# Performance work log

Measured on AMD Instinct MI355X. Metric: run time of the kernel, lower is better.

The kernel has to match this reference:

```python
import jax, jax.numpy as jnp
import numpy as np

E, H, I, T, K = 8, 2048, 768, 1024, 2


def setup_inputs() -> dict:
    key = jax.random.key(0)
    k1, k2, k3, k4, k5 = jax.random.split(key, 5)
    hidden_states = jax.random.normal(k1, (T, H), jnp.float32)
    routing_weights = jax.random.uniform(k2, (T, K), jnp.float32)
    selected_experts = jax.random.randint(k3, (T, K), 0, E, jnp.int32)
    gate_up_proj = jax.random.normal(k4, (E, H, 2 * I), jnp.float32) * 0.02
    down_proj = jax.random.normal(k5, (E, I, H), jnp.float32) * 0.02
    return {
        "hidden_states": hidden_states,
        "routing_weights": routing_weights,
        "gate_up_proj": gate_up_proj,
        "down_proj": down_proj,
        "selected_experts": selected_experts,
    }


def _grouped_gemm(x, w, expert_ids):
    # x: [N, k], w: [E, k, d], expert_ids: [N] (sorted by expert).
    # Dense-masked grouped GEMM: accumulate each expert's masked matmul.
    n = x.shape[0]
    acc0 = jnp.zeros((n, w.shape[-1]), x.dtype)

    def step(acc, ew):
        e, we = ew
        xm = jnp.where((expert_ids == e)[:, None], x, jnp.zeros((), x.dtype))
        return acc + xm @ we, None

    acc, _ = jax.lax.scan(step, acc0, (jnp.arange(w.shape[0]), w))
    return acc


def reference(hidden_states, routing_weights, gate_up_proj, down_proj, selected_experts):
    t, h = hidden_states.shape
    k = selected_experts.shape[1]
    flat = selected_experts.reshape(-1)                     # [T*K]
    sort_idx = jnp.argsort(flat)                            # stable sort by expert id (permute)
    token_idx = sort_idx // k                               # source token per permuted row
    permuted = hidden_states[token_idx]                     # [T*K, H]
    experts_sorted = flat[sort_idx]                         # [T*K]

    fc1 = _grouped_gemm(permuted, gate_up_proj, experts_sorted)   # [T*K, 2I]
    a, b = jnp.split(fc1, 2, axis=-1)
    act = jax.nn.silu(a) * b                                # npu_swiglu
    fc2 = _grouped_gemm(act, down_proj, experts_sorted)     # [T*K, H]

    inv = jnp.argsort(sort_idx)                             # unpermute map (row_ids_map)
    unperm = fc2[inv].reshape(t, k, h)                      # [T, K, H]
    return jnp.einsum('tkh,tk->th', unperm, routing_weights)
```

## Files before the change

### kernel.cpp

```cpp
#include <hip/hip_runtime.h>
#include <math.h>

#define E_  8
#define H_  2048
#define I_  768
#define T_  1024
#define K_  2
#define TK_ 2048
#define GU_ 1536

typedef __bf16 bf16x8 __attribute__((ext_vector_type(8)));
typedef float  f32x4  __attribute__((ext_vector_type(4)));

static __device__ __forceinline__ short f2bf(float f) {
  union { float f; unsigned u; } v; v.f = f;
  unsigned r = (v.u + 0x7fffu + ((v.u >> 16) & 1u)) >> 16;
  return (short)r;
}

static __device__ __forceinline__ unsigned pk2bf(float a, float b) {
  unsigned ua = __float_as_uint(a) + 0x8000u;
  unsigned ub = __float_as_uint(b) + 0x8000u;
  return __builtin_amdgcn_perm(ub, ua, 0x07060302u);
}

#define GLOAD_LDS16(g, l)                                                   \
  __builtin_amdgcn_global_load_lds(                                         \
      (const __attribute__((address_space(1))) void*)(g),                   \
      (__attribute__((address_space(3))) void*)(l), 16, 0, 0)

#define MFMA_BF16_16x16x32 __builtin_amdgcn_mfma_f32_16x16x32_bf16

static __device__ __forceinline__ bf16x8 frag_ld(const unsigned short* base,
                                                 int row, int oct) {
  return *(const bf16x8*)(base + row * 64 + ((oct ^ (row & 7)) * 8));
}

static __device__ __forceinline__ bf16x8 bfrag_ld(const unsigned short* base,
                                                  int n, int o) {
  int phys = (o ^ (n & 7) ^ (n >> 3)) & 7;
  return *(const bf16x8*)(base + n * 64 + phys * 8);
}

#define STEP(IT, G)                                                         \
  do {                                                                      \
    asm volatile("s_waitcnt vmcnt(4)" ::: "memory");                        \
    __builtin_amdgcn_s_barrier();                                           \
    __builtin_amdgcn_sched_barrier(0);                                      \
    int k1_ = ((IT) + 1 < niter ? (IT) + 1 : niter - 1) * 64;               \
    int k3_ = ((IT) + 3 < niter ? (IT) + 3 : niter - 1) * 64;               \
    issueA(cur ^ 1, k1_);                                                   \
    __builtin_amdgcn_sched_barrier(0);                                      \
    const unsigned short* a_ = &As[cur][0];                                 \
    const unsigned short* b_ = &Bs[cur][0];                                 \
    __builtin_amdgcn_s_setprio(1);                                          \
    _Pragma("unroll")                                                       \
    for (int kk = 0; kk < 2; ++kk) {                                        \
      int o = kk * 4 + qf;                                                  \
      bf16x8 af0 = frag_ld(a_, w * 32 + m,      o);                         \
      bf16x8 af1 = frag_ld(a_, w * 32 + 16 + m, o);                         \
      bf16x8 b0  = bfrag_ld(b_, m,      o);                                 \
      bf16x8 b1  = bfrag_ld(b_, 16 + m, o);                                 \
      bf16x8 b2  = bfrag_ld(b_, 32 + m, o);                                 \
      bf16x8 b3  = bfrag_ld(b_, 48 + m, o);                                 \
      acc[0][0] = MFMA_BF16_16x16x32(af0, b0, acc[0][0], 0, 0, 0);          \
      acc[0][1] = MFMA_BF16_16x16x32(af0, b1, acc[0][1], 0, 0, 0);          \
      acc[0][2] = MFMA_BF16_16x16x32(af0, b2, acc[0][2], 0, 0, 0);          \
      acc[0][3] = MFMA_BF16_16x16x32(af0, b3, acc[0][3], 0, 0, 0);          \
      acc[1][0] = MFMA_BF16_16x16x32(af1, b0, acc[1][0], 0, 0, 0);          \
      acc[1][1] = MFMA_BF16_16x16x32(af1, b1, acc[1][1], 0, 0, 0);          \
      acc[1][2] = MFMA_BF16_16x16x32(af1, b2, acc[1][2], 0, 0, 0);          \
      acc[1][3] = MFMA_BF16_16x16x32(af1, b3, acc[1][3], 0, 0, 0);          \
    }                                                                       \
    __builtin_amdgcn_s_setprio(0);                                          \
    writeB(cur ^ 1, G);                                                     \
    loadB(G, k3_);                                                          \
    asm volatile("s_waitcnt lgkmcnt(0)" ::: "memory");                      \
    __builtin_amdgcn_sched_barrier(0);                                      \
    cur ^= 1;                                                               \
  } while (0)

__global__ __launch_bounds__(256) void prep_kernel(
    const float* __restrict__ X, unsigned short* __restrict__ Xb,
    float* __restrict__ out,
    const int* __restrict__ sel, int* __restrict__ offs,
    int* __restrict__ rows, int* __restrict__ inv, int zero_out) {
  __shared__ int cnt[E_], cur[E_], loff[E_ + 1];
  if (blockIdx.x < 2048) {
    int i = blockIdx.x * 256 + threadIdx.x;
    float4 v = ((const float4*)X)[i];
    unsigned p0 = pk2bf(v.x, v.y), p1 = pk2bf(v.z, v.w);
    ((uint2*)Xb)[i] = make_uint2(p0, p1);
    if (zero_out) ((float4*)out)[i] = make_float4(0.f, 0.f, 0.f, 0.f);
    return;
  }
  int t = threadIdx.x;
  if (t < E_) { cnt[t] = 0; cur[t] = 0; }
  __syncthreads();
  for (int p = t; p < TK_; p += 256) atomicAdd(&cnt[sel[p]], 1);
  __syncthreads();
  if (t == 0) {
    int s = 0;
    for (int e = 0; e < E_; ++e) { loff[e] = s; s += cnt[e]; }
    loff[E_] = s;
  }
  __syncthreads();
  if (t <= E_) offs[t] = loff[t];
  for (int p = t; p < TK_; p += 256) {
    int e = sel[p];
    int pos = loff[e] + atomicAdd(&cur[e], 1);
    rows[pos] = p;
    inv[p] = pos;
  }
}

__global__ __launch_bounds__(256, 3) void fc1_mfma(
    const unsigned short* __restrict__ Xb, const float* __restrict__ GUP,
    const int* __restrict__ offs, const int* __restrict__ rows,
    unsigned short* __restrict__ act) {
  __shared__ __align__(16) unsigned short As[2][128 * 64];
  __shared__ __align__(16) unsigned short Bs[2][64 * 64];

  int e    = blockIdx.y >> 4;
  int rbeg = offs[e], rend = offs[e + 1];
  int row0 = rbeg + (blockIdx.y & 15) * 128;
  if (row0 >= rend) return;
  int c0 = blockIdx.x * 32;

  int tid = threadIdx.x, lane = tid & 63, w = tid >> 6;
  int rl  = lane >> 3;
  int oct = (lane & 7) ^ rl;

  const unsigned short* agp[4];
#pragma unroll
  for (int i = 0; i < 4; ++i) {
    int arow = row0 + w * 32 + i * 8 + rl;
    int aidx = arow < rend ? arow : rend - 1;
    agp[i] = Xb + (size_t)(rows[aidx] >> 1) * H_ + oct * 8;
  }
  auto issueA = [&](int buf, int k0) {
#pragma unroll
    for (int i = 0; i < 4; ++i)
      GLOAD_LDS16(agp[i] + k0, &As[buf][0] + (w * 32 + i * 8) * 64);
  };

  int kt = tid >> 4, nt = tid & 15;
  int gbase = (nt < 8) ? (c0 + nt * 4) : (I_ + c0 + (nt - 8) * 4);
  const float* gupe = GUP + (size_t)e * H_ * GU_ + gbase;

  auto loadB = [&](float4 (&vb)[4], int k0) {
#pragma unroll
    for (int i = 0; i < 4; ++i)
      vb[i] = *(const float4*)(gupe + (size_t)(k0 + kt * 4 + i) * GU_);
  };
  auto writeB = [&](int buf, const float4 (&vb)[4]) {
#pragma unroll
    for (int j = 0; j < 4; ++j) {
      int n = nt * 4 + j;
      unsigned u0 = pk2bf(((const float*)&vb[0])[j], ((const float*)&vb[1])[j]);
      unsigned u1 = pk2bf(((const float*)&vb[2])[j], ((const float*)&vb[3])[j]);
      int phys = ((kt >> 1) ^ (n & 7) ^ (n >> 3)) & 7;
      *(uint2*)(&Bs[buf][0] + n * 64 + phys * 8 + (kt & 1) * 4) =
          make_uint2(u0, u1);
    }
  };

  int m = lane & 15, qf = lane >> 4;
  f32x4 acc[2][4] = {};
  float4 vbA[4], vbB[4];

  issueA(0, 0);
  __builtin_amdgcn_sched_barrier(0);
  loadB(vbA, 0);
  writeB(0, vbA);
  loadB(vbA, 64);
  loadB(vbB, 128);
  asm volatile("s_waitcnt lgkmcnt(0)" ::: "memory");
  __builtin_amdgcn_sched_barrier(0);

  const int niter = H_ / 64;
  int cur = 0;
#pragma unroll 1
  for (int it = 0; it < niter; it += 2) {
    STEP(it,     vbA);
    STEP(it + 1, vbB);
  }
  asm volatile("s_waitcnt vmcnt(0)" ::: "memory");

#pragma unroll
  for (int mt = 0; mt < 2; ++mt)
#pragma unroll
    for (int g = 0; g < 2; ++g)
#pragma unroll
      for (int r = 0; r < 4; ++r) {
        int prow = row0 + w * 32 + mt * 16 + qf * 4 + r;
        if (prow < rend) {
          float gv = acc[mt][g][r], uv = acc[mt][g + 2][r];
          float a = gv / (1.0f + __expf(-gv)) * uv;
          act[(size_t)prow * I_ + c0 + g * 16 + m] = (unsigned short)f2bf(a);
        }
      }
}

__global__ __launch_bounds__(256, 3) void fc2_mfma(
    const unsigned short* __restrict__ act, const float* __restrict__ DWN,
    const float* __restrict__ RW,
    const int* __restrict__ offs, const int* __restrict__ rows,
    float* __restrict__ stage, float* __restrict__ out, int use_stage) {
  __shared__ __align__(16) unsigned short As[2][128 * 64];
  __shared__ __align__(16) unsigned short Bs[2][64 * 64];

  int e    = blockIdx.y >> 4;
  int rbeg = offs[e], rend = offs[e + 1];
  int row0 = rbeg + (blockIdx.y & 15) * 128;
  if (row0 >= rend) return;
  int c0 = blockIdx.x * 64;

  int tid = threadIdx.x, lane = tid & 63, w = tid >> 6;
  int rl  = lane >> 3;
  int oct = (lane & 7) ^ rl;

  const unsigned short* agp[4];
#pragma unroll
  for (int i = 0; i < 4; ++i) {
    int arow = row0 + w * 32 + i * 8 + rl;
    int aidx = arow < rend ? arow : rend - 1;
    agp[i] = act + (size_t)aidx * I_ + oct * 8;
  }
  auto issueA = [&](int buf, int k0) {
#pragma unroll
    for (int i = 0; i < 4; ++i)
      GLOAD_LDS16(agp[i] + k0, &As[buf][0] + (w * 32 + i * 8) * 64);
  };

  int kt = tid >> 4, nt = tid & 15;
  const float* dwe = DWN + (size_t)e * I_ * H_ + c0 + nt * 4;

  auto loadB = [&](float4 (&vb)[4], int k0) {
#pragma unroll
    for (int i = 0; i < 4; ++i)
      vb[i] = *(const float4*)(dwe + (size_t)(k0 + kt * 4 + i) * H_);
  };
  auto writeB = [&](int buf, const float4 (&vb)[4]) {
#pragma unroll
    for (int j = 0; j < 4; ++j) {
      int n = nt * 4 + j;
      unsigned u0 = pk2bf(((const float*)&vb[0])[j], ((const float*)&vb[1])[j]);
      unsigned u1 = pk2bf(((const float*)&vb[2])[j], ((const float*)&vb[3])[j]);
      int phys = ((kt >> 1) ^ (n & 7) ^ (n >> 3)) & 7;
      *(uint2*)(&Bs[buf][0] + n * 64 + phys * 8 + (kt & 1) * 4) =
          make_uint2(u0, u1);
    }
  };

  int m = lane & 15, qf = lane >> 4;
  f32x4 acc[2][4] = {};
  float4 vbA[4], vbB[4];

  issueA(0, 0);
  __builtin_amdgcn_sched_barrier(0);
  loadB(vbA, 0);
  writeB(0, vbA);
  loadB(vbA, 64);
  loadB(vbB, 128);
  asm volatile("s_waitcnt lgkmcnt(0)" ::: "memory");
  __builtin_amdgcn_sched_barrier(0);

  const int niter = I_ / 64;
  int cur = 0;
#pragma unroll 1
  for (int it = 0; it < niter; it += 2) {
    STEP(it,     vbA);
    STEP(it + 1, vbB);
  }
  asm volatile("s_waitcnt vmcnt(0)" ::: "memory");

#pragma unroll
  for (int mt = 0; mt < 2; ++mt)
#pragma unroll
    for (int r = 0; r < 4; ++r) {
      int prow = row0 + w * 32 + mt * 16 + qf * 4 + r;
      if (prow < rend) {
        int pair = rows[prow];
        float rw = RW[pair];
        if (use_stage) {
          float* srow = stage + (size_t)prow * H_ + c0 + m;
          srow[0]  = rw * acc[mt][0][r];
          srow[16] = rw * acc[mt][1][r];
          srow[32] = rw * acc[mt][2][r];
          srow[48] = rw * acc[mt][3][r];
        } else {
          float* orow = out + (size_t)(pair >> 1) * H_ + c0 + m;
#pragma unroll
          for (int ntile = 0; ntile < 4; ++ntile)
            atomicAdd(orow + ntile * 16, rw * acc[mt][ntile][r]);
        }
      }
    }
}

__global__ __launch_bounds__(256) void combine_kernel(
    const float* __restrict__ stage, const int* __restrict__ inv,
    float* __restrict__ out) {
  int idx = blockIdx.x * 256 + threadIdx.x;
  int t  = idx >> 9;
  int q  = idx & 511;
  int2 pp = *(const int2*)(inv + 2 * t);
  float4 a = ((const float4*)(stage + (size_t)pp.x * H_))[q];
  float4 b = ((const float4*)(stage + (size_t)pp.y * H_))[q];
  ((float4*)out)[idx] = make_float4(a.x + b.x, a.y + b.y, a.z + b.z, a.w + b.w);
}

extern "C" void kernel_launch(void* const* d_in, const int* in_sizes, int n_in,
                              void* d_out, int out_size, void* d_ws, size_t ws_size,
                              hipStream_t stream) {
  const float* X   = (const float*)d_in[0];
  const float* RW  = (const float*)d_in[1];
  const float* GUP = (const float*)d_in[2];
  const float* DWN = (const float*)d_in[3];
  const int*   SEL = (const int*)d_in[4];
  float* out = (float*)d_out;

  char* ws = (char*)d_ws;
  int* offs = (int*)ws;
  int* rows = (int*)(ws + 1024);
  int* inv  = (int*)(ws + 16384);

  const size_t stage_bytes = (size_t)TK_ * H_ * 4;
  const size_t act_bytes   = (size_t)TK_ * I_ * 2;
  const size_t need_stage  = 32768 + stage_bytes + act_bytes;

  int use_stage = (ws_size >= need_stage) ? 1 : 0;
  unsigned short *Xb, *act;
  float* stage;
  if (use_stage) {
    stage = (float*)(ws + 32768);
    Xb    = (unsigned short*)(ws + 32768);
    act   = (unsigned short*)(ws + 32768 + stage_bytes);
  } else {
    stage = (float*)(ws + 32768);
    Xb    = (unsigned short*)(ws + 32768);
    act   = (unsigned short*)(ws + 32768 + 4194304);
  }

  hipLaunchKernelGGL(prep_kernel, dim3(2049), dim3(256), 0, stream,
                     X, Xb, out, SEL, offs, rows, inv, use_stage ? 0 : 1);
  hipLaunchKernelGGL(fc1_mfma, dim3(24, 128), dim3(256), 0, stream,
                     Xb, GUP, offs, rows, act);
  hipLaunchKernelGGL(fc2_mfma, dim3(32, 128), dim3(256), 0, stream,
                     act, DWN, RW, offs, rows, stage, out, use_stage);
  if (use_stage)
    hipLaunchKernelGGL(combine_kernel, dim3(2048), dim3(256), 0, stream,
                       stage, inv, out);
}
```

Measured before the change: 251.1 us.

## Widen fc2 tile to 128 columns with single B prefetch buffer

The fc2 grouped GEMM tile grows from 128x64 to 128x128 output columns. Each block now does twice the MFMA work per A tile, which halves the reloads of activation rows across column blocks and halves the grid. The double-register B prefetch is replaced by a single 8-float4 buffer with a new step macro and a different vmcnt wait. Occupancy drops from 3 to 2 blocks per CU, and register and LDS pressure rise.

```diff
diff --git a/kernel.cpp b/kernel.cpp
--- a/kernel.cpp
+++ b/kernel.cpp
@@ -80,6 +80,38 @@
     cur ^= 1;                                                               \
   } while (0)
 
+#define STEP2(IT)                                                           \
+  do {                                                                      \
+    asm volatile("s_waitcnt vmcnt(8)" ::: "memory");                        \
+    __builtin_amdgcn_s_barrier();                                           \
+    __builtin_amdgcn_sched_barrier(0);                                      \
+    int k1_ = ((IT) + 1 < niter ? (IT) + 1 : niter - 1) * 64;               \
+    int k2_ = ((IT) + 2 < niter ? (IT) + 2 : niter - 1) * 64;               \
+    issueA(cur ^ 1, k1_);                                                   \
+    __builtin_amdgcn_sched_barrier(0);                                      \
+    const unsigned short* a_ = &As[cur][0];                                 \
+    const unsigned short* b_ = &Bs[cur][0];                                 \
+    __builtin_amdgcn_s_setprio(1);                                          \
+    _Pragma("unroll")                                                       \
+    for (int kk = 0; kk < 2; ++kk) {                                        \
+      int o = kk * 4 + qf;                                                  \
+      bf16x8 af0 = frag_ld(a_, w * 32 + m,      o);                         \
+      bf16x8 af1 = frag_ld(a_, w * 32 + 16 + m, o);                         \
+      _Pragma("unroll")                                                     \
+      for (int j = 0; j < 8; ++j) {                                         \
+        bf16x8 bj = bfrag_ld(b_, j * 16 + m, o);                            \
+        acc[0][j] = MFMA_BF16_16x16x32(af0, bj, acc[0][j], 0, 0, 0);        \
+        acc[1][j] = MFMA_BF16_16x16x32(af1, bj, acc[1][j], 0, 0, 0);        \
+      }                                                                     \
+    }                                                                       \
+    __builtin_amdgcn_s_setprio(0);                                          \
+    writeB(cur ^ 1, vb);                                                    \
+    loadB(vb, k2_);                                                         \
+    asm volatile("s_waitcnt lgkmcnt(0)" ::: "memory");                      \
+    __builtin_amdgcn_sched_barrier(0);                                      \
+    cur ^= 1;                                                               \
+  } while (0)
+
 __global__ __launch_bounds__(256) void prep_kernel(
     const float* __restrict__ X, unsigned short* __restrict__ Xb,
     float* __restrict__ out,
@@ -202,19 +234,19 @@
       }
 }
 
-__global__ __launch_bounds__(256, 3) void fc2_mfma(
+__global__ __launch_bounds__(256, 2) void fc2_mfma(
     const unsigned short* __restrict__ act, const float* __restrict__ DWN,
     const float* __restrict__ RW,
     const int* __restrict__ offs, const int* __restrict__ rows,
     float* __restrict__ stage, float* __restrict__ out, int use_stage) {
   __shared__ __align__(16) unsigned short As[2][128 * 64];
-  __shared__ __align__(16) unsigned short Bs[2][64 * 64];
+  __shared__ __align__(16) unsigned short Bs[2][128 * 64];
 
   int e    = blockIdx.y >> 4;
   int rbeg = offs[e], rend = offs[e + 1];
   int row0 = rbeg + (blockIdx.y & 15) * 128;
   if (row0 >= rend) return;
-  int c0 = blockIdx.x * 64;
+  int c0 = blockIdx.x * 128;
 
   int tid = threadIdx.x, lane = tid & 63, w = tid >> 6;
   int rl  = lane >> 3;
@@ -236,42 +268,44 @@
   int kt = tid >> 4, nt = tid & 15;
   const float* dwe = DWN + (size_t)e * I_ * H_ + c0 + nt * 4;
 
-  auto loadB = [&](float4 (&vb)[4], int k0) {
-#pragma unroll
-    for (int i = 0; i < 4; ++i)
-      vb[i] = *(const float4*)(dwe + (size_t)(k0 + kt * 4 + i) * H_);
-  };
-  auto writeB = [&](int buf, const float4 (&vb)[4]) {
-#pragma unroll
-    for (int j = 0; j < 4; ++j) {
-      int n = nt * 4 + j;
-      unsigned u0 = pk2bf(((const float*)&vb[0])[j], ((const float*)&vb[1])[j]);
-      unsigned u1 = pk2bf(((const float*)&vb[2])[j], ((const float*)&vb[3])[j]);
-      int phys = ((kt >> 1) ^ (n & 7) ^ (n >> 3)) & 7;
-      *(uint2*)(&Bs[buf][0] + n * 64 + phys * 8 + (kt & 1) * 4) =
-          make_uint2(u0, u1);
+  auto loadB = [&](float4 (&vb)[8], int k0) {
+#pragma unroll
+    for (int i = 0; i < 4; ++i) {
+      vb[i]     = *(const float4*)(dwe + (size_t)(k0 + kt * 4 + i) * H_);
+      vb[4 + i] = *(const float4*)(dwe + (size_t)(k0 + kt * 4 + i) * H_ + 64);
     }
   };
+  auto writeB = [&](int buf, const float4 (&vb)[8]) {
+#pragma unroll
+    for (int h = 0; h < 2; ++h)
+#pragma unroll
+      for (int j = 0; j < 4; ++j) {
+        int n = h * 64 + nt * 4 + j;
+        unsigned u0 = pk2bf(((const float*)&vb[h*4+0])[j], ((const float*)&vb[h*4+1])[j]);
+        unsigned u1 = pk2bf(((const float*)&vb[h*4+2])[j], ((const float*)&vb[h*4+3])[j]);
+        int phys = ((kt >> 1) ^ (n & 7) ^ (n >> 3)) & 7;
+        *(uint2*)(&Bs[buf][0] + n * 64 + phys * 8 + (kt & 1) * 4) =
+            make_uint2(u0, u1);
+      }
+  };
 
   int m = lane & 15, qf = lane >> 4;
-  f32x4 acc[2][4] = {};
-  float4 vbA[4], vbB[4];
+  f32x4 acc[2][8] = {};
+  float4 vb[8];
 
   issueA(0, 0);
   __builtin_amdgcn_sched_barrier(0);
-  loadB(vbA, 0);
-  writeB(0, vbA);
-  loadB(vbA, 64);
-  loadB(vbB, 128);
+  loadB(vb, 0);
+  writeB(0, vb);
+  loadB(vb, 64);
   asm volatile("s_waitcnt lgkmcnt(0)" ::: "memory");
   __builtin_amdgcn_sched_barrier(0);
 
   const int niter = I_ / 64;
   int cur = 0;
 #pragma unroll 1
-  for (int it = 0; it < niter; it += 2) {
-    STEP(it,     vbA);
-    STEP(it + 1, vbB);
+  for (int it = 0; it < niter; ++it) {
+    STEP2(it);
   }
   asm volatile("s_waitcnt vmcnt(0)" ::: "memory");
 
@@ -281,19 +315,17 @@
     for (int r = 0; r < 4; ++r) {
       int prow = row0 + w * 32 + mt * 16 + qf * 4 + r;
       if (prow < rend) {
-        int pair = rows[prow];
-        float rw = RW[pair];
+        int pairid = rows[prow];
+        float rw = RW[pairid];
         if (use_stage) {
           float* srow = stage + (size_t)prow * H_ + c0 + m;
-          srow[0]  = rw * acc[mt][0][r];
-          srow[16] = rw * acc[mt][1][r];
-          srow[32] = rw * acc[mt][2][r];
-          srow[48] = rw * acc[mt][3][r];
+#pragma unroll
+          for (int j = 0; j < 8; ++j) srow[j * 16] = rw * acc[mt][j][r];
         } else {
-          float* orow = out + (size_t)(pair >> 1) * H_ + c0 + m;
-#pragma unroll
-          for (int ntile = 0; ntile < 4; ++ntile)
-            atomicAdd(orow + ntile * 16, rw * acc[mt][ntile][r]);
+          float* orow = out + (size_t)(pairid >> 1) * H_ + c0 + m;
+#pragma unroll
+          for (int j = 0; j < 8; ++j)
+            atomicAdd(orow + j * 16, rw * acc[mt][j][r]);
         }
       }
     }
@@ -347,7 +379,7 @@
                      X, Xb, out, SEL, offs, rows, inv, use_stage ? 0 : 1);
   hipLaunchKernelGGL(fc1_mfma, dim3(24, 128), dim3(256), 0, stream,
                      Xb, GUP, offs, rows, act);
-  hipLaunchKernelGGL(fc2_mfma, dim3(32, 128), dim3(256), 0, stream,
+  hipLaunchKernelGGL(fc2_mfma, dim3(16, 128), dim3(256), 0, stream,
                      act, DWN, RW, offs, rows, stage, out, use_stage);
   if (use_stage)
     hipLaunchKernelGGL(combine_kernel, dim3(2048), dim3(256), 0, stream,
```

After: 254.2 us. About the same (+1.2%).

## Deepen K-tile to 128 and restructure MFMA pipeline with split A halves

Applied to the files above, without the earlier changes.

Both GEMM kernels now process a 128-wide K slice per iteration. B is staged as a 64x128 bf16 tile loaded with 8 float4s per thread and written with 16-byte LDS stores, and A is split into two 64-wide halves that are refilled right after each half's MFMAs finish. The aim is to halve the number of loop iterations and barriers and to widen the LDS writes. In exchange LDS use grows and occupancy is lowered to 2 blocks per CU, with one barrier per iteration and a single B register buffer. A redundant stage store was also added.

```diff
diff --git a/kernel.cpp b/kernel.cpp
--- a/kernel.cpp
+++ b/kernel.cpp
@@ -36,47 +36,58 @@
   return *(const bf16x8*)(base + row * 64 + ((oct ^ (row & 7)) * 8));
 }
 
-static __device__ __forceinline__ bf16x8 bfrag_ld(const unsigned short* base,
-                                                  int n, int o) {
-  int phys = (o ^ (n & 7) ^ (n >> 3)) & 7;
-  return *(const bf16x8*)(base + n * 64 + phys * 8);
-}
-
-#define STEP(IT, G)                                                         \
+static __device__ __forceinline__ bf16x8 bfrag2_ld(const unsigned short* base,
+                                                   int n, int h, int o) {
+  int phys = h * 8 + ((o ^ (n & 7) ^ (n >> 3)) & 7);
+  return *(const bf16x8*)(base + n * 128 + phys * 8);
+}
+
+#define MFMA_HALF(H)                                                        \
+  _Pragma("unroll")                                                         \
+  for (int kk = 0; kk < 2; ++kk) {                                          \
+    int o = kk * 4 + qf;                                                    \
+    bf16x8 af0 = frag_ld(&As[H][0], w * 32 + m,      o);                    \
+    bf16x8 af1 = frag_ld(&As[H][0], w * 32 + 16 + m, o);                    \
+    bf16x8 b0  = bfrag2_ld(b_, m,      (H), o);                             \
+    bf16x8 b1  = bfrag2_ld(b_, 16 + m, (H), o);                             \
+    bf16x8 b2  = bfrag2_ld(b_, 32 + m, (H), o);                             \
+    bf16x8 b3  = bfrag2_ld(b_, 48 + m, (H), o);                             \
+    acc[0][0] = MFMA_BF16_16x16x32(af0, b0, acc[0][0], 0, 0, 0);            \
+    acc[0][1] = MFMA_BF16_16x16x32(af0, b1, acc[0][1], 0, 0, 0);            \
+    acc[0][2] = MFMA_BF16_16x16x32(af0, b2, acc[0][2], 0, 0, 0);            \
+    acc[0][3] = MFMA_BF16_16x16x32(af0, b3, acc[0][3], 0, 0, 0);            \
+    acc[1][0] = MFMA_BF16_16x16x32(af1, b0, acc[1][0], 0, 0, 0);            \
+    acc[1][1] = MFMA_BF16_16x16x32(af1, b1, acc[1][1], 0, 0, 0);            \
+    acc[1][2] = MFMA_BF16_16x16x32(af1, b2, acc[1][2], 0, 0, 0);            \
+    acc[1][3] = MFMA_BF16_16x16x32(af1, b3, acc[1][3], 0, 0, 0);            \
+  }
+
+#define STEPN(IT)                                                           \
   do {                                                                      \
-    asm volatile("s_waitcnt vmcnt(4)" ::: "memory");                        \
+    int kn_ = ((IT) + 1 < niter ? (IT) + 1 : niter - 1) * 128;              \
+    int k2_ = ((IT) + 2 < niter ? (IT) + 2 : niter - 1) * 128;              \
+    const unsigned short* b_ = &Bs[cur][0];                                 \
+    asm volatile("s_waitcnt vmcnt(12)" ::: "memory");                       \
+    __builtin_amdgcn_sched_barrier(0);                                      \
+    __builtin_amdgcn_s_setprio(1);                                         \
+    MFMA_HALF(0)                                                            \
+    __builtin_amdgcn_s_setprio(0);                                         \
+    asm volatile("s_waitcnt lgkmcnt(0)" ::: "memory");                      \
+    __builtin_amdgcn_sched_barrier(0);                                      \
+    issueA(0, kn_);                                                         \
+    asm volatile("s_waitcnt vmcnt(12)" ::: "memory");                       \
+    __builtin_amdgcn_sched_barrier(0);                                      \
+    __builtin_amdgcn_s_setprio(1);                                         \
+    MFMA_HALF(1)                                                            \
+    __builtin_amdgcn_s_setprio(0);                                         \
+    asm volatile("s_waitcnt lgkmcnt(0)" ::: "memory");                      \
+    __builtin_amdgcn_sched_barrier(0);                                      \
+    issueA(1, kn_ + 64);                                                    \
+    writeB(cur ^ 1, vb);                                                    \
+    loadB(vb, k2_);                                                         \
+    asm volatile("s_waitcnt lgkmcnt(0)" ::: "memory");                      \
+    __builtin_amdgcn_sched_barrier(0);                                      \
     __builtin_amdgcn_s_barrier();                                           \
-    __builtin_amdgcn_sched_barrier(0);                                      \
-    int k1_ = ((IT) + 1 < niter ? (IT) + 1 : niter - 1) * 64;               \
-    int k3_ = ((IT) + 3 < niter ? (IT) + 3 : niter - 1) * 64;               \
-    issueA(cur ^ 1, k1_);                                                   \
-    __builtin_amdgcn_sched_barrier(0);                                      \
-    const unsigned short* a_ = &As[cur][0];                                 \
-    const unsigned short* b_ = &Bs[cur][0];                                 \
-    __builtin_amdgcn_s_setprio(1);                                          \
-    _Pragma("unroll")                                                       \
-    for (int kk = 0; kk < 2; ++kk) {                                        \
-      int o = kk * 4 + qf;                                                  \
-      bf16x8 af0 = frag_ld(a_, w * 32 + m,      o);                         \
-      bf16x8 af1 = frag_ld(a_, w * 32 + 16 + m, o);                         \
-      bf16x8 b0  = bfrag_ld(b_, m,      o);                                 \
-      bf16x8 b1  = bfrag_ld(b_, 16 + m, o);                                 \
-      bf16x8 b2  = bfrag_ld(b_, 32 + m, o);                                 \
-      bf16x8 b3  = bfrag_ld(b_, 48 + m, o);                                 \
-      acc[0][0] = MFMA_BF16_16x16x32(af0, b0, acc[0][0], 0, 0, 0);          \
-      acc[0][1] = MFMA_BF16_16x16x32(af0, b1, acc[0][1], 0, 0, 0);          \
-      acc[0][2] = MFMA_BF16_16x16x32(af0, b2, acc[0][2], 0, 0, 0);          \
-      acc[0][3] = MFMA_BF16_16x16x32(af0, b3, acc[0][3], 0, 0, 0);          \
-      acc[1][0] = MFMA_BF16_16x16x32(af1, b0, acc[1][0], 0, 0, 0);          \
-      acc[1][1] = MFMA_BF16_16x16x32(af1, b1, acc[1][1], 0, 0, 0);          \
-      acc[1][2] = MFMA_BF16_16x16x32(af1, b2, acc[1][2], 0, 0, 0);          \
-      acc[1][3] = MFMA_BF16_16x16x32(af1, b3, acc[1][3], 0, 0, 0);          \
-    }                                                                       \
-    __builtin_amdgcn_s_setprio(0);                                          \
-    writeB(cur ^ 1, G);                                                     \
-    loadB(G, k3_);                                                          \
-    asm volatile("s_waitcnt lgkmcnt(0)" ::: "memory");                      \
-    __builtin_amdgcn_sched_barrier(0);                                      \
     cur ^= 1;                                                               \
   } while (0)
 
@@ -114,12 +125,12 @@
   }
 }
 
-__global__ __launch_bounds__(256, 3) void fc1_mfma(
+__global__ __launch_bounds__(256, 2) void fc1_mfma(
     const unsigned short* __restrict__ Xb, const float* __restrict__ GUP,
     const int* __restrict__ offs, const int* __restrict__ rows,
     unsigned short* __restrict__ act) {
   __shared__ __align__(16) unsigned short As[2][128 * 64];
-  __shared__ __align__(16) unsigned short Bs[2][64 * 64];
+  __shared__ __align__(16) unsigned short Bs[2][64 * 128];
 
   int e    = blockIdx.y >> 4;
   int rbeg = offs[e], rend = offs[e + 1];
@@ -138,52 +149,55 @@
     int aidx = arow < rend ? arow : rend - 1;
     agp[i] = Xb + (size_t)(rows[aidx] >> 1) * H_ + oct * 8;
   }
-  auto issueA = [&](int buf, int k0) {
+  auto issueA = [&](int half, int k0) {
 #pragma unroll
     for (int i = 0; i < 4; ++i)
-      GLOAD_LDS16(agp[i] + k0, &As[buf][0] + (w * 32 + i * 8) * 64);
-  };
-
-  int kt = tid >> 4, nt = tid & 15;
+      GLOAD_LDS16(agp[i] + k0, &As[half][0] + (w * 32 + i * 8) * 64);
+  };
+
+  int kt8 = tid >> 4, nt = tid & 15;
   int gbase = (nt < 8) ? (c0 + nt * 4) : (I_ + c0 + (nt - 8) * 4);
   const float* gupe = GUP + (size_t)e * H_ * GU_ + gbase;
 
-  auto loadB = [&](float4 (&vb)[4], int k0) {
-#pragma unroll
-    for (int i = 0; i < 4; ++i)
-      vb[i] = *(const float4*)(gupe + (size_t)(k0 + kt * 4 + i) * GU_);
-  };
-  auto writeB = [&](int buf, const float4 (&vb)[4]) {
+  auto loadB = [&](float4 (&vb)[8], int k0) {
+#pragma unroll
+    for (int i = 0; i < 8; ++i)
+      vb[i] = *(const float4*)(gupe + (size_t)(k0 + kt8 * 8 + i) * GU_);
+  };
+  auto writeB = [&](int buf, const float4 (&vb)[8]) {
+    int h = kt8 >> 3, ko = kt8 & 7;
 #pragma unroll
     for (int j = 0; j < 4; ++j) {
       int n = nt * 4 + j;
       unsigned u0 = pk2bf(((const float*)&vb[0])[j], ((const float*)&vb[1])[j]);
       unsigned u1 = pk2bf(((const float*)&vb[2])[j], ((const float*)&vb[3])[j]);
-      int phys = ((kt >> 1) ^ (n & 7) ^ (n >> 3)) & 7;
-      *(uint2*)(&Bs[buf][0] + n * 64 + phys * 8 + (kt & 1) * 4) =
-          make_uint2(u0, u1);
+      unsigned u2 = pk2bf(((const float*)&vb[4])[j], ((const float*)&vb[5])[j]);
+      unsigned u3 = pk2bf(((const float*)&vb[6])[j], ((const float*)&vb[7])[j]);
+      int phys = h * 8 + ((ko ^ (n & 7) ^ (n >> 3)) & 7);
+      *(uint4*)(&Bs[buf][0] + n * 128 + phys * 8) = make_uint4(u0, u1, u2, u3);
     }
   };
 
   int m = lane & 15, qf = lane >> 4;
   f32x4 acc[2][4] = {};
-  float4 vbA[4], vbB[4];
-
+  float4 vb[8];
+
+  loadB(vb, 0);
+  writeB(0, vb);
+  __builtin_amdgcn_sched_barrier(0);
   issueA(0, 0);
-  __builtin_amdgcn_sched_barrier(0);
-  loadB(vbA, 0);
-  writeB(0, vbA);
-  loadB(vbA, 64);
-  loadB(vbB, 128);
+  issueA(1, 64);
+  __builtin_amdgcn_sched_barrier(0);
+  loadB(vb, 128);
   asm volatile("s_waitcnt lgkmcnt(0)" ::: "memory");
   __builtin_amdgcn_sched_barrier(0);
-
-  const int niter = H_ / 64;
+  __builtin_amdgcn_s_barrier();
+
+  const int niter = H_ / 128;
   int cur = 0;
 #pragma unroll 1
-  for (int it = 0; it < niter; it += 2) {
-    STEP(it,     vbA);
-    STEP(it + 1, vbB);
+  for (int it = 0; it < niter; ++it) {
+    STEPN(it);
   }
   asm volatile("s_waitcnt vmcnt(0)" ::: "memory");
 
@@ -202,13 +216,13 @@
       }
 }
 
-__global__ __launch_bounds__(256, 3) void fc2_mfma(
+__global__ __launch_bounds__(256, 2) void fc2_mfma(
     const unsigned short* __restrict__ act, const float* __restrict__ DWN,
     const float* __restrict__ RW,
     const int* __restrict__ offs, const int* __restrict__ rows,
     float* __restrict__ stage, float* __restrict__ out, int use_stage) {
   __shared__ __align__(16) unsigned short As[2][128 * 64];
-  __shared__ __align__(16) unsigned short Bs[2][64 * 64];
+  __shared__ __align__(16) unsigned short Bs[2][64 * 128];
 
   int e    = blockIdx.y >> 4;
   int rbeg = offs[e], rend = offs[e + 1];
@@ -227,51 +241,54 @@
     int aidx = arow < rend ? arow : rend - 1;
     agp[i] = act + (size_t)aidx * I_ + oct * 8;
   }
-  auto issueA = [&](int buf, int k0) {
+  auto issueA = [&](int half, int k0) {
 #pragma unroll
     for (int i = 0; i < 4; ++i)
-      GLOAD_LDS16(agp[i] + k0, &As[buf][0] + (w * 32 + i * 8) * 64);
-  };
-
-  int kt = tid >> 4, nt = tid & 15;
+      GLOAD_LDS16(agp[i] + k0, &As[half][0] + (w * 32 + i * 8) * 64);
+  };
+
+  int kt8 = tid >> 4, nt = tid & 15;
   const float* dwe = DWN + (size_t)e * I_ * H_ + c0 + nt * 4;
 
-  auto loadB = [&](float4 (&vb)[4], int k0) {
-#pragma unroll
-    for (int i = 0; i < 4; ++i)
-      vb[i] = *(const float4*)(dwe + (size_t)(k0 + kt * 4 + i) * H_);
-  };
-  auto writeB = [&](int buf, const float4 (&vb)[4]) {
+  auto loadB = [&](float4 (&vb)[8], int k0) {
+#pragma unroll
+    for (int i = 0; i < 8; ++i)
+      vb[i] = *(const float4*)(dwe + (size_t)(k0 + kt8 * 8 + i) * H_);
+  };
+  auto writeB = [&](int buf, const float4 (&vb)[8]) {
+    int h = kt8 >> 3, ko = kt8 & 7;
 #pragma unroll
     for (int j = 0; j < 4; ++j) {
       int n = nt * 4 + j;
       unsigned u0 = pk2bf(((const float*)&vb[0])[j], ((const float*)&vb[1])[j]);
       unsigned u1 = pk2bf(((const float*)&vb[2])[j], ((const float*)&vb[3])[j]);
-      int phys = ((kt >> 1) ^ (n & 7) ^ (n >> 3)) & 7;
-      *(uint2*)(&Bs[buf][0] + n * 64 + phys * 8 + (kt & 1) * 4) =
-          make_uint2(u0, u1);
+      unsigned u2 = pk2bf(((const float*)&vb[4])[j], ((const float*)&vb[5])[j]);
+      unsigned u3 = pk2bf(((const float*)&vb[6])[j], ((const float*)&vb[7])[j]);
+      int phys = h * 8 + ((ko ^ (n & 7) ^ (n >> 3)) & 7);
+      *(uint4*)(&Bs[buf][0] + n * 128 + phys * 8) = make_uint4(u0, u1, u2, u3);
     }
   };
 
   int m = lane & 15, qf = lane >> 4;
   f32x4 acc[2][4] = {};
-  float4 vbA[4], vbB[4];
-
+  float4 vb[8];
+
+  loadB(vb, 0);
+  writeB(0, vb);
+  __builtin_amdgcn_sched_barrier(0);
   issueA(0, 0);
-  __builtin_amdgcn_sched_barrier(0);
-  loadB(vbA, 0);
-  writeB(0, vbA);
-  loadB(vbA, 64);
-  loadB(vbB, 128);
+  issueA(1, 64);
+  __builtin_amdgcn_sched_barrier(0);
+  loadB(vb, 128);
   asm volatile("s_waitcnt lgkmcnt(0)" ::: "memory");
   __builtin_amdgcn_sched_barrier(0);
-
-  const int niter = I_ / 64;
+  __builtin_amdgcn_s_barrier();
+
+  const int niter = I_ / 128;
   int cur = 0;
 #pragma unroll 1
-  for (int it = 0; it < niter; it += 2) {
-    STEP(it,     vbA);
-    STEP(it + 1, vbB);
+  for (int it = 0; it < niter; ++it) {
+    STEPN(it);
   }
   asm volatile("s_waitcnt vmcnt(0)" ::: "memory");
 
@@ -281,16 +298,17 @@
     for (int r = 0; r < 4; ++r) {
       int prow = row0 + w * 32 + mt * 16 + qf * 4 + r;
       if (prow < rend) {
-        int pair = rows[prow];
-        float rw = RW[pair];
+        int pairid = rows[prow];
+        float rw = RW[pairid];
         if (use_stage) {
           float* srow = stage + (size_t)prow * H_ + c0 + m;
+          srow[0]  = rw * acc[0 + 0][0][r];
           srow[0]  = rw * acc[mt][0][r];
           srow[16] = rw * acc[mt][1][r];
           srow[32] = rw * acc[mt][2][r];
           srow[48] = rw * acc[mt][3][r];
         } else {
-          float* orow = out + (size_t)(pair >> 1) * H_ + c0 + m;
+          float* orow = out + (size_t)(pairid >> 1) * H_ + c0 + m;
 #pragma unroll
           for (int ntile = 0; ntile < 4; ++ntile)
             atomicAdd(orow + ntile * 16, rw * acc[mt][ntile][r]);
```

Measured after the change: 267.9 us. +6.7%, slower.
